# Performance work log

Hardware: AMD Instinct MI355X
Metric: run time of the kernel (lower is better)

Reference implementation:

```python
import jax, jax.numpy as jnp
import numpy as np

EPS = 1e-12  # layer_norm_eps

def gelu_bert(x):
    return 0.5 * x * (1.0 + jax.lax.erf(x / jnp.sqrt(2.0).astype(x.dtype)))

def sym_normalize(A):
    # D^{-1/2} A D^{-1/2} via outer-product scaling (algebraic form of diag matmuls)
    d = A.sum(-1)                      # [B,N] row sums
    dinv = jnp.power(d, -0.5)
    return A * dinv[..., :, None] * dinv[..., None, :]

def layernorm(x, g, b):
    mu = x.mean(-1, keepdims=True)
    var = ((x - mu) ** 2).mean(-1, keepdims=True)
    return (x - mu) * jax.lax.rsqrt(var + EPS) * g + b

def gcn(x, adj, w1, w2):
    x = jax.nn.relu(jnp.matmul(adj, x @ w1))   # [B,N,I]
    x = jax.nn.relu(jnp.matmul(adj, x @ w2))   # [B,N,H]
    return x

def setup_inputs() -> dict:
    B, N, H, I = 8, 1024, 768, 3072
    key = jax.random.key(0)
    ks = jax.random.split(key, 20)
    s = 0.02
    inp = {
        'nodes': jax.random.normal(ks[0], (B, N, H), jnp.float32),
        'graphs': jax.random.uniform(ks[1], (B, 2, N, N), jnp.float32),
        'gcn1_w1': jax.random.normal(ks[2], (H, I), jnp.float32) * s,
        'gcn1_w2': jax.random.normal(ks[3], (I, H), jnp.float32) * s,
        'gcn2_w1': jax.random.normal(ks[4], (H, I), jnp.float32) * s,
        'gcn2_w2': jax.random.normal(ks[5], (I, H), jnp.float32) * s,
        'exp1_w': jax.random.normal(ks[6], (H, I), jnp.float32) * s,
        'exp1_b': jnp.zeros((I,), jnp.float32),
        'col1_w': jax.random.normal(ks[7], (I, H), jnp.float32) * s,
        'col1_b': jnp.zeros((H,), jnp.float32),
        'exp2_w': jax.random.normal(ks[8], (H, I), jnp.float32) * s,
        'exp2_b': jnp.zeros((I,), jnp.float32),
        'col2_w': jax.random.normal(ks[9], (I, H), jnp.float32) * s,
        'col2_b': jnp.zeros((H,), jnp.float32),
        'gate_w': jax.random.normal(ks[10], (4 * H, H), jnp.float32) * s,
        'gate_b': jnp.zeros((H,), jnp.float32),
        'ln1_g': jnp.ones((H,), jnp.float32),
        'ln1_b': jnp.zeros((H,), jnp.float32),
        'ln2_g': jnp.ones((H,), jnp.float32),
        'ln2_b': jnp.zeros((H,), jnp.float32),
    }
    return inp

def reference(nodes, graphs, gcn1_w1, gcn1_w2, gcn2_w1, gcn2_w2,
              exp1_w, exp1_b, col1_w, col1_b, exp2_w, exp2_b, col2_w, col2_b,
              gate_w, gate_b, ln1_g, ln1_b, ln2_g, ln2_b):
    adj1 = sym_normalize(graphs[:, 0])   # [B,N,N]
    adj2 = sym_normalize(graphs[:, 1])
    g1 = gcn(nodes, adj1, gcn1_w1, gcn1_w2)  # [B,N,H]
    g2 = gcn(nodes, adj2, gcn2_w1, gcn2_w2)
    # FFN + residual + LN (dropout = identity at eval)
    g1 = gelu_bert(g1 @ exp1_w + exp1_b) @ col1_w + col1_b
    g1 = layernorm(nodes + g1, ln1_g, ln1_b)
    g2 = gelu_bert(g2 @ exp2_w + exp2_b) @ col2_w + col2_b
    g2 = layernorm(nodes + g2, ln2_g, ln2_b)
    gate_in = jnp.concatenate((g1, g2, g1 + g2, g1 - g2), axis=2)  # [B,N,4H]
    gate = jax.nn.sigmoid(gate_in @ gate_w + gate_b)
    return gate * g1 + (1.0 - gate) * g2
```

## Files before the change

### kernel.cpp

```cpp
#include <hip/hip_runtime.h>
#include <hip/hip_bf16.h>

typedef __bf16 b8v __attribute__((ext_vector_type(8)));
typedef float  f4v __attribute__((ext_vector_type(4)));
typedef unsigned long long ull;

#define AS3(p)  ((__attribute__((address_space(3))) void*)(p))
#define AS1C(p) ((const __attribute__((address_space(1))) void*)(p))

template<int EPI, int OBF, int ORIENT>
__global__ __launch_bounds__(256) void gemm_bt(
    const __hip_bfloat16* __restrict__ A,  long long sA,
    const __hip_bfloat16* __restrict__ Bt, long long sBg, long long sBb, int ldB,
    void* __restrict__ Cv, long long sC, int ldC,
    const float* __restrict__ bias0, const float* __restrict__ bias1,
    const __hip_bfloat16* __restrict__ gcat, int K)
{
  const int bz = blockIdx.z;
  A  += (long long)bz * sA;
  Bt += (long long)(bz >> 3) * sBg + (long long)(bz & 7) * sBb;
  const float* __restrict__ bias = (bz & 1) ? bias1 : bias0;

  __shared__ __hip_bfloat16 As[128 * 32];
  __shared__ __hip_bfloat16 Bs[128 * 32];

  const int tid  = threadIdx.x;
  const int lane = tid & 63;
  const int wave = tid >> 6;

  const long long m0 = (long long)blockIdx.x * 128;
  const long long n0 = (long long)blockIdx.y * 128;

  const int r  = tid >> 2;
  const int kc = (tid & 3) ^ ((r >> 2) & 3);
  const __hip_bfloat16* aSrc = A  + (m0 + r) * (long long)K   + kc * 8;
  const __hip_bfloat16* bSrc = Bt + (n0 + r) * (long long)ldB + kc * 8;

  const int wm = (wave & 1) * 64;
  const int wn = (wave >> 1) * 64;
  const int lm = lane & 15;
  const int kq = lane >> 4;

  const int sw   = (lm >> 2) & 3;
  const int aOff = (wm + lm) * 32 + (kq ^ sw) * 8;
  const int bOff = (wn + lm) * 32 + (kq ^ sw) * 8;

  f4v acc[4][4];
  const f4v fzero = {0.0f, 0.0f, 0.0f, 0.0f};
#pragma unroll
  for (int i = 0; i < 4; i++)
#pragma unroll
    for (int j = 0; j < 4; j++) acc[i][j] = fzero;

  for (int k0 = 0; k0 < K; k0 += 32) {
    __builtin_amdgcn_global_load_lds(AS1C(aSrc),                AS3(As + tid * 8),        16, 0, 0);
    __builtin_amdgcn_global_load_lds(AS1C(aSrc + 64LL * K),     AS3(As + 2048 + tid * 8), 16, 0, 0);
    __builtin_amdgcn_global_load_lds(AS1C(bSrc),                AS3(Bs + tid * 8),        16, 0, 0);
    __builtin_amdgcn_global_load_lds(AS1C(bSrc + 64LL * ldB),   AS3(Bs + 2048 + tid * 8), 16, 0, 0);
    __syncthreads();

    b8v af[4], bf[4];
#pragma unroll
    for (int i = 0; i < 4; i++) af[i] = *(const b8v*)(As + aOff + i * 16 * 32);
#pragma unroll
    for (int j = 0; j < 4; j++) bf[j] = *(const b8v*)(Bs + bOff + j * 16 * 32);

#pragma unroll
    for (int i = 0; i < 4; i++)
#pragma unroll
      for (int j = 0; j < 4; j++) {
        if constexpr (ORIENT == 0)
          acc[i][j] = __builtin_amdgcn_mfma_f32_16x16x32_bf16(bf[j], af[i], acc[i][j], 0, 0, 0);
        else
          acc[i][j] = __builtin_amdgcn_mfma_f32_16x16x32_bf16(af[i], bf[j], acc[i][j], 0, 0, 0);
      }

    __syncthreads();
    aSrc += 32; bSrc += 32;
  }

  char* Cb = (char*)Cv;

#pragma unroll
  for (int i = 0; i < 4; i++) {
#pragma unroll
    for (int j = 0; j < 4; j++) {
      float v[4];
#pragma unroll
      for (int rg = 0; rg < 4; rg++) v[rg] = acc[i][j][rg];

      if constexpr (ORIENT == 0) {
        const long long row  = m0 + wm + i * 16 + lm;
        const int       colb = (int)n0 + wn + j * 16 + kq * 4;
        if constexpr (EPI == 1) {
#pragma unroll
          for (int rg = 0; rg < 4; rg++) v[rg] = fmaxf(v[rg], 0.0f);
        }
        if constexpr (EPI == 2) {
          const float4 b4 = *(const float4*)(bias + colb);
          const float* bb = (const float*)&b4;
#pragma unroll
          for (int rg = 0; rg < 4; rg++) {
            float x = v[rg] + bb[rg];
            v[rg] = 0.5f * x * (1.0f + erff(x * 0.70710678118654752f));
          }
        }
        const long long base = bz * sC + row * (long long)ldC + colb;
        if constexpr (EPI == 3) {
          const float4 b4 = *(const float4*)(bias0 + colb);
          const float* bb = (const float*)&b4;
          union { __hip_bfloat16 h[4]; ull u; } g1, g2;
          g1.u = *(const ull*)(gcat + row * 1536 + colb);
          g2.u = *(const ull*)(gcat + row * 1536 + 768 + colb);
          float o[4];
#pragma unroll
          for (int rg = 0; rg < 4; rg++) {
            const float s = 1.0f / (1.0f + expf(-(v[rg] + bb[rg])));
            o[rg] = s * __bfloat162float(g1.h[rg]) +
                    (1.0f - s) * __bfloat162float(g2.h[rg]);
          }
          *(float4*)(Cb + base * 4) = *(const float4*)o;
        } else if constexpr (OBF) {
          union { __hip_bfloat16 h[4]; ull u; } P;
#pragma unroll
          for (int rg = 0; rg < 4; rg++) P.h[rg] = __float2bfloat16(v[rg]);
          *(ull*)(Cb + base * 2) = P.u;
        } else {
          *(float4*)(Cb + base * 4) = *(const float4*)v;
        }
      } else {
        const long long crow = n0 + wn + j * 16 + lm;
        const long long mb   = m0 + wm + i * 16 + kq * 4;
        if constexpr (EPI == 1) {
#pragma unroll
          for (int rg = 0; rg < 4; rg++) v[rg] = fmaxf(v[rg], 0.0f);
        }
        const long long base = bz * sC + crow * (long long)ldC + mb;
        if constexpr (OBF) {
          union { __hip_bfloat16 h[4]; ull u; } P;
#pragma unroll
          for (int rg = 0; rg < 4; rg++) P.h[rg] = __float2bfloat16(v[rg]);
          *(ull*)(Cb + base * 2) = P.u;
        } else {
          *(float4*)(Cb + base * 4) = *(const float4*)v;
        }
      }
    }
  }
}

__global__ __launch_bounds__(256) void rowsum_dinv(const float* __restrict__ g,
                                                   float* __restrict__ dinv)
{
  const int wave = threadIdx.x >> 6, lane = threadIdx.x & 63;
  const long long row = (long long)blockIdx.x * 4 + wave;
  const float4* p = (const float4*)(g + row * 1024);
  float s = 0.0f;
#pragma unroll
  for (int k = 0; k < 4; k++) {
    float4 v = p[lane + k * 64];
    s += v.x + v.y + v.z + v.w;
  }
#pragma unroll
  for (int o = 32; o > 0; o >>= 1) s += __shfl_down(s, o);
  if (lane == 0) dinv[row] = 1.0f / sqrtf(s);
}

__global__ __launch_bounds__(256) void scale_adj(const float* __restrict__ g,
                                                 const float* __restrict__ dinv,
                                                 __hip_bfloat16* __restrict__ out)
{
  const long long t = (long long)blockIdx.x * 256 + threadIdx.x;
  const long long e = t * 4;
  const int m = (int)(e >> 20);
  const int i = (int)((e >> 10) & 1023);
  const int j = (int)(e & 1023);
  const float4 v  = *(const float4*)(g + e);
  const float  di = dinv[m * 1024 + i];
  const float4 dj = *(const float4*)(dinv + m * 1024 + j);
  const int om = (m & 1) * 8 + (m >> 1);
  union { __hip_bfloat16 h[4]; ull u; } r;
  r.h[0] = __float2bfloat16(v.x * di * dj.x);
  r.h[1] = __float2bfloat16(v.y * di * dj.y);
  r.h[2] = __float2bfloat16(v.z * di * dj.z);
  r.h[3] = __float2bfloat16(v.w * di * dj.w);
  *(ull*)(out + ((long long)om << 20) + (long long)i * 1024 + j) = r.u;
}

template<typename TIN>
__global__ void transpose_conv(const TIN* __restrict__ in, __hip_bfloat16* __restrict__ out,
                               int R, int C, long long sIn, long long sOut)
{
  __shared__ __hip_bfloat16 tile[32][33];
  in  += (long long)blockIdx.z * sIn;
  out += (long long)blockIdx.z * sOut;
  const int c0 = blockIdx.x * 32, r0 = blockIdx.y * 32;
  const int tx = threadIdx.x, ty = threadIdx.y;
#pragma unroll
  for (int i = 0; i < 32; i += 8)
    tile[ty + i][tx] = __float2bfloat16((float)in[(long long)(r0 + ty + i) * C + c0 + tx]);
  __syncthreads();
#pragma unroll
  for (int i = 0; i < 32; i += 8)
    out[(long long)(c0 + ty + i) * R + r0 + tx] = tile[tx][ty + i];
}

__global__ __launch_bounds__(256) void ln_residual2(
    const float* __restrict__ nodes, const __hip_bfloat16* __restrict__ V,
    const float* __restrict__ colb0, const float* __restrict__ colb1,
    const float* __restrict__ lng0,  const float* __restrict__ lng1,
    const float* __restrict__ lnb0,  const float* __restrict__ lnb1,
    __hip_bfloat16* __restrict__ gcat)
{
  const long long row = blockIdx.x;
  const int g = (int)(row >> 13);
  const long long rr = row & 8191;
  const float* __restrict__ colb = g ? colb1 : colb0;
  const float* __restrict__ lng  = g ? lng1  : lng0;
  const float* __restrict__ lnb  = g ? lnb1  : lnb0;
  const int t = threadIdx.x;
  const long long nbase = rr * 768;
  const long long vbase = row * 768;
  float x[3]; float s = 0.0f, ss = 0.0f;
#pragma unroll
  for (int i = 0; i < 3; i++) {
    const int c = t + i * 256;
    const float v = nodes[nbase + c] + __bfloat162float(V[vbase + c]) + colb[c];
    x[i] = v; s += v; ss += v * v;
  }
  __shared__ float red[8];
#pragma unroll
  for (int o = 32; o > 0; o >>= 1) { s += __shfl_down(s, o); ss += __shfl_down(ss, o); }
  const int wave = t >> 6, lane = t & 63;
  if (lane == 0) { red[wave] = s; red[4 + wave] = ss; }
  __syncthreads();
  if (t == 0) {
    red[0] = red[0] + red[1] + red[2] + red[3];
    red[4] = red[4] + red[5] + red[6] + red[7];
  }
  __syncthreads();
  const float mu  = red[0] * (1.0f / 768.0f);
  float var = red[4] * (1.0f / 768.0f) - mu * mu;
  var = fmaxf(var, 0.0f);
  const float rs = rsqrtf(var + 1e-12f);
#pragma unroll
  for (int i = 0; i < 3; i++) {
    const int c = t + i * 256;
    const float y = (x[i] - mu) * rs * lng[c] + lnb[c];
    gcat[rr * 1536 + g * 768 + c] = __float2bfloat16(y);
  }
}

__global__ __launch_bounds__(256) void build_wefft(const float* __restrict__ gw,
                                                   __hip_bfloat16* __restrict__ wt)
{
  const int idx = blockIdx.x * 256 + threadIdx.x;
  const int n = idx / 1536, k = idx % 1536;
  float v;
  if (k < 768) v = gw[k * 768 + n] + gw[(1536 + k) * 768 + n] + gw[(2304 + k) * 768 + n];
  else {
    const int kk = k - 768;
    v = gw[(768 + kk) * 768 + n] + gw[(1536 + kk) * 768 + n] - gw[(2304 + kk) * 768 + n];
  }
  wt[idx] = __float2bfloat16(v);
}

extern "C" void kernel_launch(void* const* d_in, const int* in_sizes, int n_in,
                              void* d_out, int out_size, void* d_ws, size_t ws_size,
                              hipStream_t stream)
{
  const float* nodes  = (const float*)d_in[0];
  const float* graphs = (const float*)d_in[1];
  const float* gcn_w1[2] = { (const float*)d_in[2], (const float*)d_in[4] };
  const float* gcn_w2[2] = { (const float*)d_in[3], (const float*)d_in[5] };
  const float* exp_w[2]  = { (const float*)d_in[6],  (const float*)d_in[10] };
  const float* exp_b[2]  = { (const float*)d_in[7],  (const float*)d_in[11] };
  const float* col_w[2]  = { (const float*)d_in[8],  (const float*)d_in[12] };
  const float* col_b[2]  = { (const float*)d_in[9],  (const float*)d_in[13] };
  const float* gate_w = (const float*)d_in[14];
  const float* gate_b = (const float*)d_in[15];
  const float* ln_g[2] = { (const float*)d_in[16], (const float*)d_in[18] };
  const float* ln_b[2] = { (const float*)d_in[17], (const float*)d_in[19] };
  float* out = (float*)d_out;

  char* w = (char*)d_ws;
  auto alloc = [&](size_t bytes) { char* p = w; w += (bytes + 255) & ~(size_t)255; return p; };
  float*          dinv   = (float*)alloc(16384ULL * 4);
  char*           regA   = alloc(16ULL * 1024 * 1024 * 2);
  __hip_bfloat16* adj2   = (__hip_bfloat16*)regA;
  __hip_bfloat16* Gcat   = (__hip_bfloat16*)regA;
  __hip_bfloat16* wefft  = (__hip_bfloat16*)alloc(768ULL * 1536 * 2);
  __hip_bfloat16* bufA2  = (__hip_bfloat16*)alloc(16ULL * 1024 * 768 * 2);
  char*           regD   = alloc(16ULL * 1024 * 768 * 2);
  __hip_bfloat16* Xt     = (__hip_bfloat16*)regD;
  __hip_bfloat16* bufB2  = (__hip_bfloat16*)regD;
  __hip_bfloat16* X12    = (__hip_bfloat16*)alloc(2ULL * 8192 * 3072 * 2);
  __hip_bfloat16* wgt1   = (__hip_bfloat16*)alloc(2ULL * 3072 * 768 * 2);
  __hip_bfloat16* wgt2   = (__hip_bfloat16*)alloc(2ULL * 768 * 3072 * 2);

  const long long sW1 = 3072LL * 768;
  const long long sW2 = 768LL * 3072;
  const long long sNM = 1024LL * 768;
  const long long sBig = 8192LL * 3072;

  rowsum_dinv<<<4096, 256, 0, stream>>>(graphs, dinv);
  transpose_conv<float><<<dim3(24, 32, 8), dim3(32, 8), 0, stream>>>(
      nodes, Xt, 1024, 768, 1024LL * 768, 768LL * 1024);
  build_wefft<<<4608, 256, 0, stream>>>(gate_w, wefft);
  scale_adj<<<16384, 256, 0, stream>>>(graphs, dinv, adj2);
  for (int g = 0; g < 2; g++) {
    transpose_conv<float><<<dim3(96, 24, 1), dim3(32, 8), 0, stream>>>(
        gcn_w1[g], wgt1 + g * sW1, 768, 3072, 0, 0);
    transpose_conv<float><<<dim3(24, 96, 1), dim3(32, 8), 0, stream>>>(
        gcn_w2[g], wgt2 + g * sW2, 3072, 768, 0, 0);
  }

  gemm_bt<0, 1, 0><<<dim3(8, 6, 16), 256, 0, stream>>>(
      adj2, 1LL << 20, Xt, 0, sNM, 1024, bufA2, sNM, 768,
      nullptr, nullptr, nullptr, 1024);
  gemm_bt<1, 1, 0><<<dim3(64, 24, 2), 256, 0, stream>>>(
      bufA2, 8192LL * 768, wgt1, 0, sW1, 768, X12, sBig, 3072,
      nullptr, nullptr, nullptr, 768);
  gemm_bt<0, 1, 1><<<dim3(64, 6, 2), 256, 0, stream>>>(
      X12, sBig, wgt2, 0, sW2, 3072, bufA2, 768LL * 8192, 8192,
      nullptr, nullptr, nullptr, 3072);
  for (int g = 0; g < 2; g++) {
    transpose_conv<float><<<dim3(96, 24, 1), dim3(32, 8), 0, stream>>>(
        exp_w[g], wgt1 + g * sW1, 768, 3072, 0, 0);
    transpose_conv<float><<<dim3(24, 96, 1), dim3(32, 8), 0, stream>>>(
        col_w[g], wgt2 + g * sW2, 3072, 768, 0, 0);
  }
  gemm_bt<1, 1, 0><<<dim3(8, 6, 16), 256, 0, stream>>>(
      adj2, 1LL << 20, bufA2, 768LL * 8192, 1024, 8192, bufB2, sNM, 768,
      nullptr, nullptr, nullptr, 1024);
  gemm_bt<2, 1, 0><<<dim3(64, 24, 2), 256, 0, stream>>>(
      bufB2, 8192LL * 768, wgt1, 0, sW1, 768, X12, sBig, 3072,
      exp_b[0], exp_b[1], nullptr, 768);
  gemm_bt<0, 1, 0><<<dim3(64, 6, 2), 256, 0, stream>>>(
      X12, sBig, wgt2, 0, sW2, 3072, bufA2, 8192LL * 768, 768,
      nullptr, nullptr, nullptr, 3072);
  ln_residual2<<<16384, 256, 0, stream>>>(
      nodes, bufA2, col_b[0], col_b[1], ln_g[0], ln_g[1], ln_b[0], ln_b[1], Gcat);
  gemm_bt<3, 0, 0><<<dim3(64, 6, 1), 256, 0, stream>>>(
      Gcat, 0, wefft, 0, 0, 1536, out, 0, 768,
      gate_b, nullptr, Gcat, 1536);
}
```

Before: 866.2 us.

## Prefetch next K tile during MFMA and process two M tiles per block

```diff
diff --git a/kernel.cpp b/kernel.cpp
--- a/kernel.cpp
+++ b/kernel.cpp
@@ -8,7 +8,7 @@
 #define AS3(p)  ((__attribute__((address_space(3))) void*)(p))
 #define AS1C(p) ((const __attribute__((address_space(1))) void*)(p))
 
-template<int EPI, int OBF, int ORIENT>
+template<int EPI, int OBF, int ORIENT, int MP>
 __global__ __launch_bounds__(256) void gemm_bt(
     const __hip_bfloat16* __restrict__ A,  long long sA,
     const __hip_bfloat16* __restrict__ Bt, long long sBg, long long sBb, int ldB,
@@ -28,13 +28,13 @@
   const int lane = tid & 63;
   const int wave = tid >> 6;
 
-  const long long m0 = (long long)blockIdx.x * 128;
-  const long long n0 = (long long)blockIdx.y * 128;
+  const long long mBase = (long long)blockIdx.x * (MP * 128);
+  const long long n0    = (long long)blockIdx.y * 128;
 
   const int r  = tid >> 2;
   const int kc = (tid & 3) ^ ((r >> 2) & 3);
-  const __hip_bfloat16* aSrc = A  + (m0 + r) * (long long)K   + kc * 8;
-  const __hip_bfloat16* bSrc = Bt + (n0 + r) * (long long)ldB + kc * 8;
+  const __hip_bfloat16* aRow = A  + (mBase + r) * (long long)K   + kc * 8;
+  const __hip_bfloat16* bRow = Bt + (n0 + r)    * (long long)ldB + kc * 8;
 
   const int wm = (wave & 1) * 64;
   const int wn = (wave >> 1) * 64;
@@ -45,104 +45,118 @@
   const int aOff = (wm + lm) * 32 + (kq ^ sw) * 8;
   const int bOff = (wn + lm) * 32 + (kq ^ sw) * 8;
 
-  f4v acc[4][4];
+  auto stage = [&](long long aoff, int k0) {
+    const __hip_bfloat16* a = aRow + aoff + k0;
+    const __hip_bfloat16* b = bRow + k0;
+    __builtin_amdgcn_global_load_lds(AS1C(a),              AS3(As + tid * 8),        16, 0, 0);
+    __builtin_amdgcn_global_load_lds(AS1C(a + 64LL * K),   AS3(As + 2048 + tid * 8), 16, 0, 0);
+    __builtin_amdgcn_global_load_lds(AS1C(b),              AS3(Bs + tid * 8),        16, 0, 0);
+    __builtin_amdgcn_global_load_lds(AS1C(b + 64LL * ldB), AS3(Bs + 2048 + tid * 8), 16, 0, 0);
+  };
+
+  stage(0, 0);
+
   const f4v fzero = {0.0f, 0.0f, 0.0f, 0.0f};
-#pragma unroll
-  for (int i = 0; i < 4; i++)
-#pragma unroll
-    for (int j = 0; j < 4; j++) acc[i][j] = fzero;
-
-  for (int k0 = 0; k0 < K; k0 += 32) {
-    __builtin_amdgcn_global_load_lds(AS1C(aSrc),                AS3(As + tid * 8),        16, 0, 0);
-    __builtin_amdgcn_global_load_lds(AS1C(aSrc + 64LL * K),     AS3(As + 2048 + tid * 8), 16, 0, 0);
-    __builtin_amdgcn_global_load_lds(AS1C(bSrc),                AS3(Bs + tid * 8),        16, 0, 0);
-    __builtin_amdgcn_global_load_lds(AS1C(bSrc + 64LL * ldB),   AS3(Bs + 2048 + tid * 8), 16, 0, 0);
-    __syncthreads();
-
-    b8v af[4], bf[4];
-#pragma unroll
-    for (int i = 0; i < 4; i++) af[i] = *(const b8v*)(As + aOff + i * 16 * 32);
-#pragma unroll
-    for (int j = 0; j < 4; j++) bf[j] = *(const b8v*)(Bs + bOff + j * 16 * 32);
-
+  char* Cb = (char*)Cv;
+
+  for (int p = 0; p < MP; ++p) {
+    const long long aoff = (long long)p * 128 * K;
+
+    f4v acc[4][4];
 #pragma unroll
     for (int i = 0; i < 4; i++)
 #pragma unroll
+      for (int j = 0; j < 4; j++) acc[i][j] = fzero;
+
+    for (int k0 = 0; k0 < K; k0 += 32) {
+      __syncthreads();
+
+      b8v af[4], bf[4];
+#pragma unroll
+      for (int i = 0; i < 4; i++) af[i] = *(const b8v*)(As + aOff + i * 16 * 32);
+#pragma unroll
+      for (int j = 0; j < 4; j++) bf[j] = *(const b8v*)(Bs + bOff + j * 16 * 32);
+
+      __syncthreads();
+
+      if (k0 + 32 < K)            stage(aoff, k0 + 32);
+      else if (MP > 1 && p + 1 < MP) stage(aoff + 128LL * K, 0);
+
+#pragma unroll
+      for (int i = 0; i < 4; i++)
+#pragma unroll
+        for (int j = 0; j < 4; j++) {
+          if constexpr (ORIENT == 0)
+            acc[i][j] = __builtin_amdgcn_mfma_f32_16x16x32_bf16(bf[j], af[i], acc[i][j], 0, 0, 0);
+          else
+            acc[i][j] = __builtin_amdgcn_mfma_f32_16x16x32_bf16(af[i], bf[j], acc[i][j], 0, 0, 0);
+        }
+    }
+
+    const long long m0 = mBase + (long long)p * 128;
+#pragma unroll
+    for (int i = 0; i < 4; i++) {
+#pragma unroll
       for (int j = 0; j < 4; j++) {
-        if constexpr (ORIENT == 0)
-          acc[i][j] = __builtin_amdgcn_mfma_f32_16x16x32_bf16(bf[j], af[i], acc[i][j], 0, 0, 0);
-        else
-          acc[i][j] = __builtin_amdgcn_mfma_f32_16x16x32_bf16(af[i], bf[j], acc[i][j], 0, 0, 0);
-      }
-
-    __syncthreads();
-    aSrc += 32; bSrc += 32;
-  }
-
-  char* Cb = (char*)Cv;
-
-#pragma unroll
-  for (int i = 0; i < 4; i++) {
-#pragma unroll
-    for (int j = 0; j < 4; j++) {
-      float v[4];
-#pragma unroll
-      for (int rg = 0; rg < 4; rg++) v[rg] = acc[i][j][rg];
-
-      if constexpr (ORIENT == 0) {
-        const long long row  = m0 + wm + i * 16 + lm;
-        const int       colb = (int)n0 + wn + j * 16 + kq * 4;
-        if constexpr (EPI == 1) {
-#pragma unroll
-          for (int rg = 0; rg < 4; rg++) v[rg] = fmaxf(v[rg], 0.0f);
-        }
-        if constexpr (EPI == 2) {
-          const float4 b4 = *(const float4*)(bias + colb);
-          const float* bb = (const float*)&b4;
-#pragma unroll
-          for (int rg = 0; rg < 4; rg++) {
-            float x = v[rg] + bb[rg];
-            v[rg] = 0.5f * x * (1.0f + erff(x * 0.70710678118654752f));
-          }
-        }
-        const long long base = bz * sC + row * (long long)ldC + colb;
-        if constexpr (EPI == 3) {
-          const float4 b4 = *(const float4*)(bias0 + colb);
-          const float* bb = (const float*)&b4;
-          union { __hip_bfloat16 h[4]; ull u; } g1, g2;
-          g1.u = *(const ull*)(gcat + row * 1536 + colb);
-          g2.u = *(const ull*)(gcat + row * 1536 + 768 + colb);
-          float o[4];
-#pragma unroll
-          for (int rg = 0; rg < 4; rg++) {
-            const float s = 1.0f / (1.0f + expf(-(v[rg] + bb[rg])));
-            o[rg] = s * __bfloat162float(g1.h[rg]) +
-                    (1.0f - s) * __bfloat162float(g2.h[rg]);
-          }
-          *(float4*)(Cb + base * 4) = *(const float4*)o;
-        } else if constexpr (OBF) {
-          union { __hip_bfloat16 h[4]; ull u; } P;
-#pragma unroll
-          for (int rg = 0; rg < 4; rg++) P.h[rg] = __float2bfloat16(v[rg]);
-          *(ull*)(Cb + base * 2) = P.u;
+        float v[4];
+#pragma unroll
+        for (int rg = 0; rg < 4; rg++) v[rg] = acc[i][j][rg];
+
+        if constexpr (ORIENT == 0) {
+          const long long row  = m0 + wm + i * 16 + lm;
+          const int       colb = (int)n0 + wn + j * 16 + kq * 4;
+          if constexpr (EPI == 1) {
+#pragma unroll
+            for (int rg = 0; rg < 4; rg++) v[rg] = fmaxf(v[rg], 0.0f);
+          }
+          if constexpr (EPI == 2) {
+            const float4 b4 = *(const float4*)(bias + colb);
+            const float* bb = (const float*)&b4;
+#pragma unroll
+            for (int rg = 0; rg < 4; rg++) {
+              float x = v[rg] + bb[rg];
+              v[rg] = 0.5f * x * (1.0f + erff(x * 0.70710678118654752f));
+            }
+          }
+          const long long base = bz * sC + row * (long long)ldC + colb;
+          if constexpr (EPI == 3) {
+            const float4 b4 = *(const float4*)(bias0 + colb);
+            const float* bb = (const float*)&b4;
+            union { __hip_bfloat16 h[4]; ull u; } g1, g2;
+            g1.u = *(const ull*)(gcat + row * 1536 + colb);
+            g2.u = *(const ull*)(gcat + row * 1536 + 768 + colb);
+            float o[4];
+#pragma unroll
+            for (int rg = 0; rg < 4; rg++) {
+              const float s = 1.0f / (1.0f + expf(-(v[rg] + bb[rg])));
+              o[rg] = s * __bfloat162float(g1.h[rg]) +
+                      (1.0f - s) * __bfloat162float(g2.h[rg]);
+            }
+            *(float4*)(Cb + base * 4) = *(const float4*)o;
+          } else if constexpr (OBF) {
+            union { __hip_bfloat16 h[4]; ull u; } P;
+#pragma unroll
+            for (int rg = 0; rg < 4; rg++) P.h[rg] = __float2bfloat16(v[rg]);
+            *(ull*)(Cb + base * 2) = P.u;
+          } else {
+            *(float4*)(Cb + base * 4) = *(const float4*)v;
+          }
         } else {
-          *(float4*)(Cb + base * 4) = *(const float4*)v;
-        }
-      } else {
-        const long long crow = n0 + wn + j * 16 + lm;
-        const long long mb   = m0 + wm + i * 16 + kq * 4;
-        if constexpr (EPI == 1) {
-#pragma unroll
-          for (int rg = 0; rg < 4; rg++) v[rg] = fmaxf(v[rg], 0.0f);
-        }
-        const long long base = bz * sC + crow * (long long)ldC + mb;
-        if constexpr (OBF) {
-          union { __hip_bfloat16 h[4]; ull u; } P;
-#pragma unroll
-          for (int rg = 0; rg < 4; rg++) P.h[rg] = __float2bfloat16(v[rg]);
-          *(ull*)(Cb + base * 2) = P.u;
-        } else {
-          *(float4*)(Cb + base * 4) = *(const float4*)v;
+          const long long crow = n0 + wn + j * 16 + lm;
+          const long long mb   = m0 + wm + i * 16 + kq * 4;
+          if constexpr (EPI == 1) {
+#pragma unroll
+            for (int rg = 0; rg < 4; rg++) v[rg] = fmaxf(v[rg], 0.0f);
+          }
+          const long long base = bz * sC + crow * (long long)ldC + mb;
+          if constexpr (OBF) {
+            union { __hip_bfloat16 h[4]; ull u; } P;
+#pragma unroll
+            for (int rg = 0; rg < 4; rg++) P.h[rg] = __float2bfloat16(v[rg]);
+            *(ull*)(Cb + base * 2) = P.u;
+          } else {
+            *(float4*)(Cb + base * 4) = *(const float4*)v;
+          }
         }
       }
     }
@@ -315,13 +329,13 @@
         gcn_w2[g], wgt2 + g * sW2, 3072, 768, 0, 0);
   }
 
-  gemm_bt<0, 1, 0><<<dim3(8, 6, 16), 256, 0, stream>>>(
+  gemm_bt<0, 1, 0, 1><<<dim3(8, 6, 16), 256, 0, stream>>>(
       adj2, 1LL << 20, Xt, 0, sNM, 1024, bufA2, sNM, 768,
       nullptr, nullptr, nullptr, 1024);
-  gemm_bt<1, 1, 0><<<dim3(64, 24, 2), 256, 0, stream>>>(
+  gemm_bt<1, 1, 0, 2><<<dim3(32, 24, 2), 256, 0, stream>>>(
       bufA2, 8192LL * 768, wgt1, 0, sW1, 768, X12, sBig, 3072,
       nullptr, nullptr, nullptr, 768);
-  gemm_bt<0, 1, 1><<<dim3(64, 6, 2), 256, 0, stream>>>(
+  gemm_bt<0, 1, 1, 1><<<dim3(64, 6, 2), 256, 0, stream>>>(
       X12, sBig, wgt2, 0, sW2, 3072, bufA2, 768LL * 8192, 8192,
       nullptr, nullptr, nullptr, 3072);
   for (int g = 0; g < 2; g++) {
@@ -330,18 +344,18 @@
     transpose_conv<float><<<dim3(24, 96, 1), dim3(32, 8), 0, stream>>>(
         col_w[g], wgt2 + g * sW2, 3072, 768, 0, 0);
   }
-  gemm_bt<1, 1, 0><<<dim3(8, 6, 16), 256, 0, stream>>>(
+  gemm_bt<1, 1, 0, 1><<<dim3(8, 6, 16), 256, 0, stream>>>(
       adj2, 1LL << 20, bufA2, 768LL * 8192, 1024, 8192, bufB2, sNM, 768,
       nullptr, nullptr, nullptr, 1024);
-  gemm_bt<2, 1, 0><<<dim3(64, 24, 2), 256, 0, stream>>>(
+  gemm_bt<2, 1, 0, 2><<<dim3(32, 24, 2), 256, 0, stream>>>(
       bufB2, 8192LL * 768, wgt1, 0, sW1, 768, X12, sBig, 3072,
       exp_b[0], exp_b[1], nullptr, 768);
-  gemm_bt<0, 1, 0><<<dim3(64, 6, 2), 256, 0, stream>>>(
+  gemm_bt<0, 1, 0, 1><<<dim3(64, 6, 2), 256, 0, stream>>>(
       X12, sBig, wgt2, 0, sW2, 3072, bufA2, 8192LL * 768, 768,
       nullptr, nullptr, nullptr, 3072);
   ln_residual2<<<16384, 256, 0, stream>>>(
       nodes, bufA2, col_b[0], col_b[1], ln_g[0], ln_g[1], ln_b[0], ln_b[1], Gcat);
-  gemm_bt<3, 0, 0><<<dim3(64, 6, 1), 256, 0, stream>>>(
+  gemm_bt<3, 0, 0, 1><<<dim3(64, 6, 1), 256, 0, stream>>>(
       Gcat, 0, wefft, 0, 0, 1536, out, 0, 768,
       gate_b, nullptr, Gcat, 1536);
 }
```

After: 808.2 us. 1.07x faster.
